# Kernel tuning notes

Measured on AMD Instinct MI355X. Metric: run time of the kernel, lower is better.

Reference implementation:

```python
import jax, jax.numpy as jnp
import numpy as np

N, D, H, E = 4096, 512, 8, 131072
DH = D // H
EPS = 1e-5
NEG = -1e9


def layer_norm(x, w, b):
    m = jnp.mean(x, axis=-1, keepdims=True)
    v = jnp.mean((x - m) ** 2, axis=-1, keepdims=True)
    return (x - m) * jax.lax.rsqrt(v + EPS) * w + b


def setup_inputs() -> dict:
    key = jax.random.key(0)
    ks = jax.random.split(key, 10)
    s = 0.02
    return {
        "x": jax.random.normal(ks[0], (N, D), dtype=jnp.float32),
        "edge_index": jax.random.randint(ks[1], (2, E), 0, N, dtype=jnp.int64),
        "ln1_w": jnp.ones((D,), jnp.float32),
        "ln1_b": jnp.zeros((D,), jnp.float32),
        "w_in": jax.random.normal(ks[2], (3 * D, D), jnp.float32) * s,
        "b_in": jnp.zeros((3 * D,), jnp.float32),
        "w_out": jax.random.normal(ks[3], (D, D), jnp.float32) * s,
        "b_out": jnp.zeros((D,), jnp.float32),
        "ln2_w": jnp.ones((D,), jnp.float32),
        "ln2_b": jnp.zeros((D,), jnp.float32),
        "w1": jax.random.normal(ks[4], (4 * D, D), jnp.float32) * s,
        "b1": jnp.zeros((4 * D,), jnp.float32),
        "w2": jax.random.normal(ks[5], (D, 4 * D), jnp.float32) * s,
        "b2": jnp.zeros((D,), jnp.float32),
    }


def reference(x, edge_index, ln1_w, ln1_b, w_in, b_in, w_out, b_out,
              ln2_w, ln2_b, w1, b1, w2, b2):
    n = x.shape[0]
    # adjacency mask: allowed where edge exists or on diagonal
    adj = jnp.zeros((n, n), dtype=bool)
    adj = adj.at[edge_index[0], edge_index[1]].set(True)
    adj = adj.at[jnp.arange(n), jnp.arange(n)].set(True)
    add_mask = jnp.where(adj, 0.0, NEG).astype(x.dtype)  # [n, n]

    xn = layer_norm(x, ln1_w, ln1_b)
    qkv = xn @ w_in.T + b_in  # [n, 3D]
    q, k, v = jnp.split(qkv, 3, axis=-1)
    # [n, D] -> [H, n, DH]
    q = q.reshape(n, H, DH).transpose(1, 0, 2)
    k = k.reshape(n, H, DH).transpose(1, 0, 2)
    v = v.reshape(n, H, DH).transpose(1, 0, 2)
    scores = jnp.einsum("hqd,hkd->hqk", q, k) / jnp.sqrt(jnp.asarray(DH, x.dtype))
    scores = scores + add_mask[None]
    attn = jax.nn.softmax(scores, axis=-1)
    o = jnp.einsum("hqk,hkd->hqd", attn, v)  # [H, n, DH]
    o = o.transpose(1, 0, 2).reshape(n, D)
    attn_out = o @ w_out.T + b_out

    x = x + attn_out  # residual (dropout=0 / eval)
    xm = layer_norm(x, ln2_w, ln2_b)
    mlp = jax.nn.relu(xm @ w1.T + b1) @ w2.T + b2
    return x + mlp
```

## Files before the change

kernel.cpp:

```cpp
#include <hip/hip_runtime.h>

#define NN 4096
#define DD 512
#define HH 8
#define DHH 64

typedef __attribute__((ext_vector_type(8))) __bf16 bfrag;
typedef __attribute__((ext_vector_type(8))) short short8;
typedef __attribute__((ext_vector_type(8))) unsigned short ushort8v;
typedef __attribute__((ext_vector_type(4))) float f32x4;
typedef unsigned int uint32;

#define GLOAD16(gp, lp)                                                        \
    __builtin_amdgcn_global_load_lds(                                          \
        (const __attribute__((address_space(1))) unsigned int*)(gp),           \
        (__attribute__((address_space(3))) unsigned int*)(lp), 16, 0, 0)

__device__ __forceinline__ unsigned short f2b(float f) {
    unsigned int u = __builtin_bit_cast(unsigned int, f);
    unsigned int r = 0x7fffu + ((u >> 16) & 1u);
    return (unsigned short)((u + r) >> 16);
}

__device__ __forceinline__ float b2f(unsigned short u) {
    return __builtin_bit_cast(float, (unsigned int)u << 16);
}

__device__ __forceinline__ float fexp2(float x) {
#if __has_builtin(__builtin_amdgcn_exp2f)
    return __builtin_amdgcn_exp2f(x);
#else
    return exp2f(x);
#endif
}

__device__ __forceinline__ void load_edge(const void* ei, int E, int i, int is32,
                                          int& r, int& c) {
    if (is32) {
        const int* p = (const int*)ei;
        r = p[i]; c = p[E + i];
    } else {
        const long long* p = (const long long*)ei;
        r = (int)p[i]; c = (int)p[E + i];
    }
}

__device__ __forceinline__ void ln_row_body(const float* __restrict__ x,
                                            const float* __restrict__ w,
                                            const float* __restrict__ b,
                                            unsigned short* __restrict__ out,
                                            int row, int tid) {
    float2 v = reinterpret_cast<const float2*>(x + (size_t)row * DD)[tid];
    float s = v.x + v.y;
    float s2 = v.x * v.x + v.y * v.y;
#pragma unroll
    for (int d = 1; d < 64; d <<= 1) {
        s += __shfl_xor(s, d);
        s2 += __shfl_xor(s2, d);
    }
    __shared__ float red[8];
    if ((tid & 63) == 0) { red[tid >> 6] = s; red[4 + (tid >> 6)] = s2; }
    __syncthreads();
    s = red[0] + red[1] + red[2] + red[3];
    s2 = red[4] + red[5] + red[6] + red[7];
    const float mean = s * (1.f / DD);
    const float var = fmaxf(s2 * (1.f / DD) - mean * mean, 0.f);
    const float rs = rsqrtf(var + 1e-5f);
    const int c = tid * 2;
    out[(size_t)row * DD + c]     = f2b((v.x - mean) * rs * w[c] + b[c]);
    out[(size_t)row * DD + c + 1] = f2b((v.y - mean) * rs * w[c + 1] + b[c + 1]);
}

__global__ __launch_bounds__(256) void ln_rows(const float* __restrict__ x,
                                               const float* __restrict__ w,
                                               const float* __restrict__ b,
                                               unsigned short* __restrict__ out) {
    ln_row_body(x, w, b, out, blockIdx.x, threadIdx.x);
}

#define W_IN_N 786432
#define W_OUT_N 262144
#define W1_N 1048576
#define W2_N 1048576
#define CVT_BLKS 3072
#define LN_BLKS 4096
__global__ __launch_bounds__(256) void prologue(
    const float* __restrict__ w_in, const float* __restrict__ w_out,
    const float* __restrict__ w1, const float* __restrict__ w2,
    unsigned short* __restrict__ o_in, unsigned short* __restrict__ o_out,
    unsigned short* __restrict__ o1, unsigned short* __restrict__ o2,
    const float* __restrict__ x, const float* __restrict__ ln1w,
    const float* __restrict__ ln1b, unsigned short* __restrict__ xn,
    const void* __restrict__ ei, uint32* __restrict__ mask, int E) {
    const int bb = blockIdx.x;
    if (bb < CVT_BLKS) {
        int idx = (bb * 256 + threadIdx.x) * 4;
        const float* src;
        unsigned short* dst;
        int off;
        if (idx < W_IN_N) { src = w_in; dst = o_in; off = idx; }
        else if (idx < W_IN_N + W_OUT_N) { src = w_out; dst = o_out; off = idx - W_IN_N; }
        else if (idx < W_IN_N + W_OUT_N + W1_N) { src = w1; dst = o1; off = idx - (W_IN_N + W_OUT_N); }
        else { src = w2; dst = o2; off = idx - (W_IN_N + W_OUT_N + W1_N); }
        float4 v = *reinterpret_cast<const float4*>(src + off);
        ushort4 o;
        o.x = f2b(v.x); o.y = f2b(v.y); o.z = f2b(v.z); o.w = f2b(v.w);
        *reinterpret_cast<ushort4*>(dst + off) = o;
    } else if (bb < CVT_BLKS + LN_BLKS) {
        ln_row_body(x, ln1w, ln1b, xn, bb - CVT_BLKS, threadIdx.x);
    } else {
        __shared__ int s_any;
        if (threadIdx.x == 0) s_any = 0;
        __syncthreads();
        if (((const int*)ei)[2 * threadIdx.x + 1] != 0) atomicOr(&s_any, 1);
        __syncthreads();
        const int is32 = s_any;
        const int tid = (bb - (CVT_BLKS + LN_BLKS)) * 256 + threadIdx.x;
        const int total = E + NN;
        if (tid < total) {
            int r, c;
            if (tid < E) load_edge(ei, E, tid, is32, r, c);
            else { r = tid - E; c = r; }
            atomicOr(&mask[r * 128 + (c >> 5)], 1u << (c & 31));
        }
    }
}

template <int BM, int BN, int EPI>
__global__ __launch_bounds__(256) void gemm_swz(const unsigned short* __restrict__ A,
                                                const unsigned short* __restrict__ B,
                                                int K,
                                                const float* __restrict__ bias,
                                                const float* __restrict__ resid,
                                                float* __restrict__ out_f,
                                                unsigned short* __restrict__ out_b,
                                                float* __restrict__ q_out,
                                                unsigned short* __restrict__ k_out,
                                                unsigned short* __restrict__ v_out) {
    constexpr int MR = BM / 32;
    constexpr int NR = BN / 32;
    __shared__ __align__(16) unsigned short a_lds[BM * 64];
    __shared__ __align__(16) unsigned short b_lds[BN * 64];
    const int tid = threadIdx.x;
    const int lane = tid & 63;
    const int wave = tid >> 6;
    const int wm = wave >> 1, wn = wave & 1;
    const int wgid = blockIdx.x;
    const int tm = wgid % (NN / BM);
    const int tn = wgid / (NN / BM);

    f32x4 acc[MR][NR];
#pragma unroll
    for (int mi = 0; mi < MR; ++mi)
#pragma unroll
        for (int ni = 0; ni < NR; ++ni) acc[mi][ni] = (f32x4){0.f, 0.f, 0.f, 0.f};

    const int srow = lane >> 3;
    const int sswz = ((lane & 7) ^ srow) << 3;
    const unsigned short* a_src = A + (size_t)(tm * BM + srow) * K + sswz;
    const unsigned short* b_src = B + (size_t)(tn * BN + srow) * K + sswz;

    for (int k0 = 0; k0 < K; k0 += 64) {
        __syncthreads();
#pragma unroll
        for (int i = 0; i < BM / 32; ++i) {
            const int c = wave * (BM / 32) + i;
            GLOAD16(a_src + (size_t)c * 8 * K + k0, a_lds + c * 512);
        }
#pragma unroll
        for (int i = 0; i < BN / 32; ++i) {
            const int c = wave * (BN / 32) + i;
            GLOAD16(b_src + (size_t)c * 8 * K + k0, b_lds + c * 512);
        }
        __syncthreads();
#pragma unroll
        for (int ks = 0; ks < 2; ++ks) {
            const int cswz = (((lane >> 4) + ks * 4) ^ (lane & 7)) << 3;
            const int rl = lane & 15;
            bfrag af[MR], bfr[NR];
#pragma unroll
            for (int mi = 0; mi < MR; ++mi)
                af[mi] = *reinterpret_cast<const bfrag*>(
                    &a_lds[(wm * (BM / 2) + mi * 16 + rl) * 64 + cswz]);
#pragma unroll
            for (int ni = 0; ni < NR; ++ni)
                bfr[ni] = *reinterpret_cast<const bfrag*>(
                    &b_lds[(wn * (BN / 2) + ni * 16 + rl) * 64 + cswz]);
#pragma unroll
            for (int mi = 0; mi < MR; ++mi)
#pragma unroll
                for (int ni = 0; ni < NR; ++ni)
                    acc[mi][ni] = __builtin_amdgcn_mfma_f32_16x16x32_bf16(
                        af[mi], bfr[ni], acc[mi][ni], 0, 0, 0);
        }
    }

    const int r0 = (lane >> 4) << 2;
    const int cl = lane & 15;
#pragma unroll
    for (int mi = 0; mi < MR; ++mi) {
#pragma unroll
        for (int ni = 0; ni < NR; ++ni) {
#pragma unroll
            for (int r = 0; r < 4; ++r) {
                int gr = tm * BM + wm * (BM / 2) + mi * 16 + r0 + r;
                int gc = tn * BN + wn * (BN / 2) + ni * 16 + cl;
                float v = acc[mi][ni][r] + bias[gc];
                if (EPI == 0) {
                    if (gc < 512) {
                        q_out[(size_t)gr * 512 + gc] = v * 0.18033688011112042f;
                    } else if (gc < 1024) {
                        k_out[(size_t)gr * 512 + (gc - 512)] = f2b(v);
                    } else {
                        v_out[(size_t)gr * 512 + (gc - 1024)] = f2b(v);
                    }
                } else if (EPI == 1) {
                    out_f[(size_t)gr * 512 + gc] =
                        v + resid[(size_t)gr * 512 + gc];
                } else {
                    out_b[(size_t)gr * 2048 + gc] = f2b(fmaxf(v, 0.f));
                }
            }
        }
    }
}

__global__ __launch_bounds__(256) void attn_sparse(const float* __restrict__ qf,
                                                   const unsigned short* __restrict__ kb,
                                                   const unsigned short* __restrict__ vb,
                                                   const uint32* __restrict__ mask,
                                                   unsigned short* __restrict__ o_buf) {
    __shared__ int s_cols[4][1024];
    __shared__ int s_cnt[4];
    const int lane = threadIdx.x & 63;
    const int wid = threadIdx.x >> 6;
    const int q = blockIdx.x * 4 + wid;

    if (lane == 0) s_cnt[wid] = 0;
    uint32 w0 = mask[q * 128 + lane];
    uint32 w1 = mask[q * 128 + 64 + lane];
    const int base0 = lane * 32, base1 = (64 + lane) * 32;
    while (w0) {
        int b = __builtin_ctz(w0);
        w0 &= w0 - 1;
        int pos = atomicAdd(&s_cnt[wid], 1);
        s_cols[wid][pos & 1023] = base0 + b;
    }
    while (w1) {
        int b = __builtin_ctz(w1);
        w1 &= w1 - 1;
        int pos = atomicAdd(&s_cnt[wid], 1);
        s_cols[wid][pos & 1023] = base1 + b;
    }
    const int cnt = min(s_cnt[wid], 1024);

    const float4* qp = reinterpret_cast<const float4*>(qf + (size_t)q * DD + lane * 8);
    const float4 q0 = qp[0], q1 = qp[1];

    float m_run = -3.0e38f, l_run = 0.f;
    float oa[8];
#pragma unroll
    for (int i = 0; i < 8; ++i) oa[i] = 0.f;

    for (int j0 = 0; j0 < cnt; j0 += 8) {
        float s_arr[8];
        int col_arr[8];
#pragma unroll
        for (int u = 0; u < 8; ++u) {
            const int idx = j0 + u;
            const bool act = idx < cnt;
            const int col = s_cols[wid][act ? idx : 0];
            col_arr[u] = col;
            ushort8v kq = *reinterpret_cast<const ushort8v*>(
                kb + (size_t)col * DD + lane * 8);
            float d = q0.x * b2f(kq[0]);
            d = fmaf(q0.y, b2f(kq[1]), d);
            d = fmaf(q0.z, b2f(kq[2]), d);
            d = fmaf(q0.w, b2f(kq[3]), d);
            d = fmaf(q1.x, b2f(kq[4]), d);
            d = fmaf(q1.y, b2f(kq[5]), d);
            d = fmaf(q1.z, b2f(kq[6]), d);
            d = fmaf(q1.w, b2f(kq[7]), d);
            d += __shfl_xor(d, 1);
            d += __shfl_xor(d, 2);
            d += __shfl_xor(d, 4);
            s_arr[u] = act ? d : -3.0e38f;
        }
        float mloc = fmaxf(fmaxf(fmaxf(s_arr[0], s_arr[1]), fmaxf(s_arr[2], s_arr[3])),
                           fmaxf(fmaxf(s_arr[4], s_arr[5]), fmaxf(s_arr[6], s_arr[7])));
        if (mloc > m_run) {
            const float alpha = fexp2(m_run - mloc);
            l_run *= alpha;
#pragma unroll
            for (int i = 0; i < 8; ++i) oa[i] *= alpha;
            m_run = mloc;
        }
#pragma unroll
        for (int u = 0; u < 8; ++u) {
            const float p = fexp2(s_arr[u] - m_run);
            l_run += p;
            ushort8v vq = *reinterpret_cast<const ushort8v*>(
                vb + (size_t)col_arr[u] * DD + lane * 8);
#pragma unroll
            for (int i = 0; i < 8; ++i) oa[i] = fmaf(p, b2f(vq[i]), oa[i]);
        }
    }

    const float rl = 1.f / l_run;
    ushort8v ov;
#pragma unroll
    for (int i = 0; i < 8; ++i) ov[i] = f2b(oa[i] * rl);
    *reinterpret_cast<ushort8v*>(o_buf + (size_t)q * DD + lane * 8) = ov;
}

extern "C" void kernel_launch(void* const* d_in, const int* in_sizes, int n_in,
                              void* d_out, int out_size, void* d_ws, size_t ws_size,
                              hipStream_t stream) {
    const float* x = (const float*)d_in[0];
    const void* ei = d_in[1];
    const float* ln1w = (const float*)d_in[2];
    const float* ln1b = (const float*)d_in[3];
    const float* w_in = (const float*)d_in[4];
    const float* b_in = (const float*)d_in[5];
    const float* w_out = (const float*)d_in[6];
    const float* b_out = (const float*)d_in[7];
    const float* ln2w = (const float*)d_in[8];
    const float* ln2b = (const float*)d_in[9];
    const float* w1 = (const float*)d_in[10];
    const float* b1 = (const float*)d_in[11];
    const float* w2 = (const float*)d_in[12];
    const float* b2 = (const float*)d_in[13];
    float* out = (float*)d_out;
    const int E = in_sizes[1] / 2;

    char* ws = (char*)d_ws;
    size_t off = 0;
    auto alloc = [&](size_t bytes) -> void* {
        void* p = ws + off;
        off = (off + bytes + 255) & ~(size_t)255;
        return p;
    };
    uint32* mask1 = (uint32*)alloc((size_t)NN * 128 * 4);
    unsigned short* w_in_b = (unsigned short*)alloc((size_t)1536 * 512 * 2);
    unsigned short* w_out_b = (unsigned short*)alloc((size_t)512 * 512 * 2);
    unsigned short* w1_b = (unsigned short*)alloc((size_t)2048 * 512 * 2);
    unsigned short* w2_b = (unsigned short*)alloc((size_t)512 * 2048 * 2);
    unsigned short* xn = (unsigned short*)alloc((size_t)NN * DD * 2);
    float* q_f = (float*)alloc((size_t)NN * DD * 4);
    unsigned short* k_b = (unsigned short*)alloc((size_t)NN * DD * 2);
    unsigned short* v_b = (unsigned short*)alloc((size_t)NN * DD * 2);
    unsigned short* o_buf = (unsigned short*)alloc((size_t)NN * DD * 2);
    float* x1 = (float*)alloc((size_t)NN * DD * 4);
    unsigned short* xm = (unsigned short*)alloc((size_t)NN * DD * 2);
    unsigned short* h_buf = (unsigned short*)q_f;

    hipMemsetAsync(mask1, 0, (size_t)NN * 128 * 4, stream);

    const int adj_blks = (E + NN + 255) / 256;
    prologue<<<CVT_BLKS + LN_BLKS + adj_blks, 256, 0, stream>>>(
        w_in, w_out, w1, w2, w_in_b, w_out_b, w1_b, w2_b,
        x, ln1w, ln1b, xn, ei, mask1, E);

    gemm_swz<128, 64, 0><<<32 * 24, 256, 0, stream>>>(
        xn, w_in_b, 512, b_in, nullptr, nullptr, nullptr, q_f, k_b, v_b);
    attn_sparse<<<NN / 4, 256, 0, stream>>>(q_f, k_b, v_b, mask1, o_buf);
    gemm_swz<64, 64, 1><<<64 * 8, 256, 0, stream>>>(
        o_buf, w_out_b, 512, b_out, x, x1, nullptr, nullptr, nullptr, nullptr);
    ln_rows<<<NN, 256, 0, stream>>>(x1, ln2w, ln2b, xm);
    gemm_swz<128, 128, 2><<<32 * 16, 256, 0, stream>>>(
        xm, w1_b, 512, b1, nullptr, nullptr, h_buf, nullptr, nullptr, nullptr);
    gemm_swz<64, 64, 1><<<64 * 8, 256, 0, stream>>>(
        h_buf, w2_b, 2048, b2, x1, out, nullptr, nullptr, nullptr, nullptr);
}
```

Before: 111.5 us.

## Double-buffer GEMM LDS tiles and use one wave per row for LayerNorm

The GEMM kernel now double-buffers its A and B shared-memory tiles. It issues the next k-tile's direct-to-LDS loads before computing the current one and syncs with explicit vmcnt waits and s_barrier, so global load latency overlaps the MFMA work. LayerNorm is rewritten so each wave handles a whole row with float4 loads and a 16-byte store, which removes the cross-wave shared-memory reduction and __syncthreads and cuts the block count by four. The cost is double the GEMM LDS footprint, which may lower occupancy, and hand-written waitcnt values that must match the number of loads issued.

```diff
diff --git a/kernel.cpp b/kernel.cpp
--- a/kernel.cpp
+++ b/kernel.cpp
@@ -15,6 +15,15 @@
     __builtin_amdgcn_global_load_lds(                                          \
         (const __attribute__((address_space(1))) unsigned int*)(gp),           \
         (__attribute__((address_space(3))) unsigned int*)(lp), 16, 0, 0)
+
+template <int N>
+__device__ __forceinline__ void waitcnt_vm() {
+    if constexpr (N == 0) asm volatile("s_waitcnt vmcnt(0)" ::: "memory");
+    else if constexpr (N == 4) asm volatile("s_waitcnt vmcnt(4)" ::: "memory");
+    else if constexpr (N == 6) asm volatile("s_waitcnt vmcnt(6)" ::: "memory");
+    else if constexpr (N == 8) asm volatile("s_waitcnt vmcnt(8)" ::: "memory");
+    else static_assert(N == 0, "unsupported vmcnt literal");
+}
 
 __device__ __forceinline__ unsigned short f2b(float f) {
     unsigned int u = __builtin_bit_cast(unsigned int, f);
@@ -45,37 +54,44 @@
     }
 }
 
-__device__ __forceinline__ void ln_row_body(const float* __restrict__ x,
+__device__ __forceinline__ void ln_row_wave(const float* __restrict__ x,
                                             const float* __restrict__ w,
                                             const float* __restrict__ b,
                                             unsigned short* __restrict__ out,
-                                            int row, int tid) {
-    float2 v = reinterpret_cast<const float2*>(x + (size_t)row * DD)[tid];
-    float s = v.x + v.y;
-    float s2 = v.x * v.x + v.y * v.y;
+                                            int row, int lane) {
+    const float4* xp = reinterpret_cast<const float4*>(x + (size_t)row * DD + lane * 8);
+    const float4 v0 = xp[0], v1 = xp[1];
+    float s  = (v0.x + v0.y) + (v0.z + v0.w) + (v1.x + v1.y) + (v1.z + v1.w);
+    float s2 = v0.x * v0.x + v0.y * v0.y + v0.z * v0.z + v0.w * v0.w +
+               v1.x * v1.x + v1.y * v1.y + v1.z * v1.z + v1.w * v1.w;
 #pragma unroll
     for (int d = 1; d < 64; d <<= 1) {
         s += __shfl_xor(s, d);
         s2 += __shfl_xor(s2, d);
     }
-    __shared__ float red[8];
-    if ((tid & 63) == 0) { red[tid >> 6] = s; red[4 + (tid >> 6)] = s2; }
-    __syncthreads();
-    s = red[0] + red[1] + red[2] + red[3];
-    s2 = red[4] + red[5] + red[6] + red[7];
     const float mean = s * (1.f / DD);
     const float var = fmaxf(s2 * (1.f / DD) - mean * mean, 0.f);
     const float rs = rsqrtf(var + 1e-5f);
-    const int c = tid * 2;
-    out[(size_t)row * DD + c]     = f2b((v.x - mean) * rs * w[c] + b[c]);
-    out[(size_t)row * DD + c + 1] = f2b((v.y - mean) * rs * w[c + 1] + b[c + 1]);
+    const float4* wp = reinterpret_cast<const float4*>(w + lane * 8);
+    const float4* bp = reinterpret_cast<const float4*>(b + lane * 8);
+    const float4 w0 = wp[0], w1 = wp[1], b0 = bp[0], b1 = bp[1];
+    ushort8v o;
+    o[0] = f2b((v0.x - mean) * rs * w0.x + b0.x);
+    o[1] = f2b((v0.y - mean) * rs * w0.y + b0.y);
+    o[2] = f2b((v0.z - mean) * rs * w0.z + b0.z);
+    o[3] = f2b((v0.w - mean) * rs * w0.w + b0.w);
+    o[4] = f2b((v1.x - mean) * rs * w1.x + b1.x);
+    o[5] = f2b((v1.y - mean) * rs * w1.y + b1.y);
+    o[6] = f2b((v1.z - mean) * rs * w1.z + b1.z);
+    o[7] = f2b((v1.w - mean) * rs * w1.w + b1.w);
+    *reinterpret_cast<ushort8v*>(out + (size_t)row * DD + lane * 8) = o;
 }
 
 __global__ __launch_bounds__(256) void ln_rows(const float* __restrict__ x,
                                                const float* __restrict__ w,
                                                const float* __restrict__ b,
                                                unsigned short* __restrict__ out) {
-    ln_row_body(x, w, b, out, blockIdx.x, threadIdx.x);
+    ln_row_wave(x, w, b, out, blockIdx.x * 4 + (threadIdx.x >> 6), threadIdx.x & 63);
 }
 
 #define W_IN_N 786432
@@ -83,7 +99,7 @@
 #define W1_N 1048576
 #define W2_N 1048576
 #define CVT_BLKS 3072
-#define LN_BLKS 4096
+#define LN_BLKS 1024
 __global__ __launch_bounds__(256) void prologue(
     const float* __restrict__ w_in, const float* __restrict__ w_out,
     const float* __restrict__ w1, const float* __restrict__ w2,
@@ -107,7 +123,8 @@
         o.x = f2b(v.x); o.y = f2b(v.y); o.z = f2b(v.z); o.w = f2b(v.w);
         *reinterpret_cast<ushort4*>(dst + off) = o;
     } else if (bb < CVT_BLKS + LN_BLKS) {
-        ln_row_body(x, ln1w, ln1b, xn, bb - CVT_BLKS, threadIdx.x);
+        ln_row_wave(x, ln1w, ln1b, xn,
+                    (bb - CVT_BLKS) * 4 + (threadIdx.x >> 6), threadIdx.x & 63);
     } else {
         __shared__ int s_any;
         if (threadIdx.x == 0) s_any = 0;
@@ -139,8 +156,10 @@
                                                 unsigned short* __restrict__ v_out) {
     constexpr int MR = BM / 32;
     constexpr int NR = BN / 32;
-    __shared__ __align__(16) unsigned short a_lds[BM * 64];
-    __shared__ __align__(16) unsigned short b_lds[BN * 64];
+    constexpr int LA = BM / 32;
+    constexpr int LB = BN / 32;
+    __shared__ __align__(16) unsigned short a_lds[2 * BM * 64];
+    __shared__ __align__(16) unsigned short b_lds[2 * BN * 64];
     const int tid = threadIdx.x;
     const int lane = tid & 63;
     const int wave = tid >> 6;
@@ -160,19 +179,35 @@
     const unsigned short* a_src = A + (size_t)(tm * BM + srow) * K + sswz;
     const unsigned short* b_src = B + (size_t)(tn * BN + srow) * K + sswz;
 
-    for (int k0 = 0; k0 < K; k0 += 64) {
-        __syncthreads();
-#pragma unroll
-        for (int i = 0; i < BM / 32; ++i) {
-            const int c = wave * (BM / 32) + i;
-            GLOAD16(a_src + (size_t)c * 8 * K + k0, a_lds + c * 512);
-        }
-#pragma unroll
-        for (int i = 0; i < BN / 32; ++i) {
-            const int c = wave * (BN / 32) + i;
-            GLOAD16(b_src + (size_t)c * 8 * K + k0, b_lds + c * 512);
-        }
-        __syncthreads();
+    auto stage = [&](int k0, int buf) {
+        unsigned short* al = a_lds + buf * (BM * 64);
+        unsigned short* bl = b_lds + buf * (BN * 64);
+#pragma unroll
+        for (int i = 0; i < LA; ++i) {
+            const int c = wave * LA + i;
+            GLOAD16(a_src + (size_t)c * 8 * K + k0, al + c * 512);
+        }
+#pragma unroll
+        for (int i = 0; i < LB; ++i) {
+            const int c = wave * LB + i;
+            GLOAD16(b_src + (size_t)c * 8 * K + k0, bl + c * 512);
+        }
+    };
+
+    stage(0, 0);
+    const int NT = K >> 6;
+    for (int t = 0; t < NT; ++t) {
+        const int cur = t & 1;
+        if (t + 1 < NT) {
+            stage((t + 1) << 6, cur ^ 1);
+            waitcnt_vm<LA + LB>();
+        } else {
+            waitcnt_vm<0>();
+        }
+        __builtin_amdgcn_s_barrier();
+        asm volatile("" ::: "memory");
+        const unsigned short* al = a_lds + cur * (BM * 64);
+        const unsigned short* bl = b_lds + cur * (BN * 64);
 #pragma unroll
         for (int ks = 0; ks < 2; ++ks) {
             const int cswz = (((lane >> 4) + ks * 4) ^ (lane & 7)) << 3;
@@ -181,11 +216,11 @@
 #pragma unroll
             for (int mi = 0; mi < MR; ++mi)
                 af[mi] = *reinterpret_cast<const bfrag*>(
-                    &a_lds[(wm * (BM / 2) + mi * 16 + rl) * 64 + cswz]);
+                    &al[(wm * (BM / 2) + mi * 16 + rl) * 64 + cswz]);
 #pragma unroll
             for (int ni = 0; ni < NR; ++ni)
                 bfr[ni] = *reinterpret_cast<const bfrag*>(
-                    &b_lds[(wn * (BN / 2) + ni * 16 + rl) * 64 + cswz]);
+                    &bl[(wn * (BN / 2) + ni * 16 + rl) * 64 + cswz]);
 #pragma unroll
             for (int mi = 0; mi < MR; ++mi)
 #pragma unroll
@@ -193,6 +228,8 @@
                     acc[mi][ni] = __builtin_amdgcn_mfma_f32_16x16x32_bf16(
                         af[mi], bfr[ni], acc[mi][ni], 0, 0, 0);
         }
+        asm volatile("" ::: "memory");
+        __builtin_amdgcn_s_barrier();
     }
 
     const int r0 = (lane >> 4) << 2;
@@ -366,7 +403,7 @@
     attn_sparse<<<NN / 4, 256, 0, stream>>>(q_f, k_b, v_b, mask1, o_buf);
     gemm_swz<64, 64, 1><<<64 * 8, 256, 0, stream>>>(
         o_buf, w_out_b, 512, b_out, x, x1, nullptr, nullptr, nullptr, nullptr);
-    ln_rows<<<NN, 256, 0, stream>>>(x1, ln2w, ln2b, xm);
+    ln_rows<<<NN / 4, 256, 0, stream>>>(x1, ln2w, ln2b, xm);
     gemm_swz<128, 128, 2><<<32 * 16, 256, 0, stream>>>(
         xm, w1_b, 512, b1, nullptr, nullptr, h_buf, nullptr, nullptr, nullptr);
     gemm_swz<64, 64, 1><<<64 * 8, 256, 0, stream>>>(
```

Result: faster. 106.1 us (-4.8%).
